# Kernel optimization log

Measured on AMD Instinct MI355X. Metric: run time of the kernel, lower is better.

Reference implementation:

```python
import jax, jax.numpy as jnp
import numpy as np

RHO, MU, DT = 1.0, 0.1, 4.0
AX_X, AX_Y = -1, -2  # x = last axis, y = second-to-last


def first_derivative(f, ax, scheme):
    # unit grid spacing; boundary wrap is irrelevant since [1:-1,1:-1] is sliced off
    if scheme == 'left':
        return f - jnp.roll(f, 1, ax)
    if scheme == 'right':
        return jnp.roll(f, -1, ax) - f
    return 0.5 * (jnp.roll(f, -1, ax) - jnp.roll(f, 1, ax))  # central


def vel_map(f, ax, side):
    # staggered-grid interpolation of velocity to neighboring face
    if side == 'left':
        return 0.5 * (f + jnp.roll(f, 1, ax))
    return 0.5 * (f + jnp.roll(f, -1, ax))


def laplacian(f):
    return (jnp.roll(f, 1, AX_X) + jnp.roll(f, -1, AX_X)
            + jnp.roll(f, 1, AX_Y) + jnp.roll(f, -1, AX_Y) - 4.0 * f)


def setup_inputs() -> dict:
    key = jax.random.key(0)
    k1, k2, k3, k4 = jax.random.split(key, 4)
    B, H, W = 8, 1024, 1024
    return {
        'v_old': jax.random.normal(k1, (B, 2, H, W), dtype=jnp.float32),
        'v_new': jax.random.normal(k2, (B, 2, H, W), dtype=jnp.float32),
        'p_new': jax.random.normal(k3, (B, 1, H, W), dtype=jnp.float32),
        'flow_mask_mac': jax.random.randint(k4, (B, 1, H, W), 0, 2).astype(jnp.int32),
    }


def reference(v_old, v_new, p_new, flow_mask_mac):
    mask = flow_mask_mac.astype(v_old.dtype)
    v = 0.5 * (v_new + v_old)  # integration == 'imex'

    u_old, w_old = v_old[:, 0:1], v_old[:, 1:2]
    u_new, w_new = v_new[:, 0:1], v_new[:, 1:2]
    u, w = v[:, 0:1], v[:, 1:2]

    # x-momentum residual (channel 1)
    res_x = mask * (RHO * ((w_new - w_old) / DT
                           + w * first_derivative(w, AX_X, 'central')
                           + 0.5 * (vel_map(u, AX_X, 'left') * first_derivative(w, AX_Y, 'left')
                                    + vel_map(u, AX_X, 'right') * first_derivative(w, AX_Y, 'right')))
                    + first_derivative(p_new, AX_X, 'left')
                    - MU * laplacian(w))

    # y-momentum residual (channel 0)
    res_y = mask * (RHO * ((u_new - u_old) / DT
                           + u * first_derivative(u, AX_Y, 'central')
                           + 0.5 * (vel_map(w, AX_Y, 'left') * first_derivative(u, AX_X, 'left')
                                    + vel_map(w, AX_Y, 'right') * first_derivative(u, AX_X, 'right')))
                    + first_derivative(p_new, AX_Y, 'left')
                    - MU * laplacian(u))

    loss_x = jnp.mean(jnp.square(res_x)[:, :, 1:-1, 1:-1], axis=(1, 2, 3))
    loss_y = jnp.mean(jnp.square(res_y)[:, :, 1:-1, 1:-1], axis=(1, 2, 3))
    return loss_x + loss_y  # shape [B]
```

## Files before the change

### kernel.cpp

```cpp
#include <hip/hip_runtime.h>


#define NS_H 1024
#define NS_W 1024
#define RPB 2
#define PAIRS ((NS_H - 2) / RPB)
#define PARTS_PER_B PAIRS

__device__ __forceinline__ float4 ld4(const float* p) { return *(const float4*)p; }
__device__ __forceinline__ float4 avg4(float4 a, float4 b) {
    return make_float4(0.5f*(a.x+b.x), 0.5f*(a.y+b.y), 0.5f*(a.z+b.z), 0.5f*(a.w+b.w));
}
__device__ __forceinline__ float4 sub4(float4 a, float4 b) {
    return make_float4(a.x-b.x, a.y-b.y, a.z-b.z, a.w-b.w);
}

__global__ __launch_bounds__(256, 3) void ns_loss_partial(
    const float* __restrict__ v_old,
    const float* __restrict__ v_new,
    const float* __restrict__ p,
    const int*   __restrict__ mask,
    float* __restrict__ ws)
{
    const int blk = blockIdx.x;
    const int b   = blk / PAIRS;
    const int pr  = blk % PAIRS;
    const int y   = 1 + pr * RPB;

    const size_t hw = (size_t)NS_H * NS_W;
    const float* uo = v_old + (size_t)b * 2 * hw;
    const float* wo = uo + hw;
    const float* un = v_new + (size_t)b * 2 * hw;
    const float* wn = un + hw;
    const float* pb = p    + (size_t)b * hw;
    const int*   mb = mask + (size_t)b * hw;

    const int tid  = (int)threadIdx.x;
    const int lane = tid & 63;
    const int x0   = tid * 4;
    const bool has_r = (x0 + 4 < NS_W);
    const bool seamL = (lane == 0) && (x0 > 0);
    const bool seamR = (lane == 63) && has_r;

    const int rm  = (y - 1) * NS_W;
    const int rc  = y * NS_W;
    const int rp  = rc + NS_W;
    const int rpp = rp + NS_W;

    float4 un_m = ld4(un + rm  + x0), uo_m = ld4(uo + rm  + x0);
    float4 un_c = ld4(un + rc  + x0), uo_c = ld4(uo + rc  + x0);
    float4 un_p = ld4(un + rp  + x0), uo_p = ld4(uo + rp  + x0);
    float4 un_q = ld4(un + rpp + x0), uo_q = ld4(uo + rpp + x0);
    float4 wn_m = ld4(wn + rm  + x0), wo_m = ld4(wo + rm  + x0);
    float4 wn_c = ld4(wn + rc  + x0), wo_c = ld4(wo + rc  + x0);
    float4 wn_p = ld4(wn + rp  + x0), wo_p = ld4(wo + rp  + x0);
    float4 wn_q = ld4(wn + rpp + x0), wo_q = ld4(wo + rpp + x0);
    float4 p_m4 = ld4(pb + rm + x0);
    float4 p_c4 = ld4(pb + rc + x0);
    float4 p_p4 = ld4(pb + rp + x0);
    int4   m_c4 = *(const int4*)(mb + rc + x0);
    int4   m_p4 = *(const int4*)(mb + rp + x0);

    float4 u_m = avg4(un_m, uo_m), u_c = avg4(un_c, uo_c);
    float4 u_p = avg4(un_p, uo_p), u_q = avg4(un_q, uo_q);
    float4 w_m = avg4(wn_m, wo_m), w_c = avg4(wn_c, wo_c);
    float4 w_p = avg4(wn_p, wo_p), w_q = avg4(wn_q, wo_q);
    float4 du_c = sub4(un_c, uo_c), du_p = sub4(un_p, uo_p);
    float4 dw_c = sub4(wn_c, wo_c), dw_p = sub4(wn_p, wo_p);

    float ul_c = __shfl_up(u_c.w, 1), wl_c = __shfl_up(w_c.w, 1);
    float ul_p = __shfl_up(u_p.w, 1), wl_p = __shfl_up(w_p.w, 1);
    float pl_c = __shfl_up(p_c4.w, 1), pl_p = __shfl_up(p_p4.w, 1);
    if (seamL) {
        ul_c = 0.5f * (un[rc + x0 - 1] + uo[rc + x0 - 1]);
        wl_c = 0.5f * (wn[rc + x0 - 1] + wo[rc + x0 - 1]);
        ul_p = 0.5f * (un[rp + x0 - 1] + uo[rp + x0 - 1]);
        wl_p = 0.5f * (wn[rp + x0 - 1] + wo[rp + x0 - 1]);
        pl_c = pb[rc + x0 - 1];
        pl_p = pb[rp + x0 - 1];
    }
    float ur_c = __shfl_down(u_c.x, 1), wr_c = __shfl_down(w_c.x, 1);
    float ur_p = __shfl_down(u_p.x, 1), wr_p = __shfl_down(w_p.x, 1);
    if (seamR) {
        ur_c = 0.5f * (un[rc + x0 + 4] + uo[rc + x0 + 4]);
        wr_c = 0.5f * (wn[rc + x0 + 4] + wo[rc + x0 + 4]);
        ur_p = 0.5f * (un[rp + x0 + 4] + uo[rp + x0 + 4]);
        wr_p = 0.5f * (wn[rp + x0 + 4] + wo[rp + x0 + 4]);
    }
    if (!has_r) { ur_c = 0.f; wr_c = 0.f; ur_p = 0.f; wr_p = 0.f; }

    float acc = 0.f;

    {
        const float uc[6]  = {ul_c, u_c.x, u_c.y, u_c.z, u_c.w, ur_c};
        const float wcv[6] = {wl_c, w_c.x, w_c.y, w_c.z, w_c.w, wr_c};
        const float uym[4] = {u_m.x, u_m.y, u_m.z, u_m.w};
        const float uyp[4] = {u_p.x, u_p.y, u_p.z, u_p.w};
        const float wym[4] = {w_m.x, w_m.y, w_m.z, w_m.w};
        const float wyp[4] = {w_p.x, w_p.y, w_p.z, w_p.w};
        const float du[4]  = {du_c.x, du_c.y, du_c.z, du_c.w};
        const float dw[4]  = {dw_c.x, dw_c.y, dw_c.z, dw_c.w};
        const float pcv[5] = {pl_c, p_c4.x, p_c4.y, p_c4.z, p_c4.w};
        const float pym[4] = {p_m4.x, p_m4.y, p_m4.z, p_m4.w};
        const int   mm[4]  = {m_c4.x, m_c4.y, m_c4.z, m_c4.w};

        #pragma unroll
        for (int j = 0; j < 4; ++j) {
            const int x = x0 + j;
            const float m = (x >= 1 && x <= NS_W - 2) ? (float)mm[j] : 0.f;
            const float u_cc = uc[j+1],  u_xm = uc[j],  u_xp = uc[j+2];
            const float w_cc = wcv[j+1], w_xm = wcv[j], w_xp = wcv[j+2];

            float res_x =
                dw[j] * 0.25f
              + w_cc * 0.5f * (w_xp - w_xm)
              + 0.5f * ( 0.5f * (u_cc + u_xm) * (w_cc   - wym[j])
                       + 0.5f * (u_cc + u_xp) * (wyp[j] - w_cc  ) )
              + (pcv[j+1] - pcv[j])
              - 0.1f * (w_xm + w_xp + wym[j] + wyp[j] - 4.f * w_cc);

            float res_y =
                du[j] * 0.25f
              + u_cc * 0.5f * (uyp[j] - uym[j])
              + 0.5f * ( 0.5f * (w_cc + wym[j]) * (u_cc - u_xm)
                       + 0.5f * (w_cc + wyp[j]) * (u_xp - u_cc) )
              + (pcv[j+1] - pym[j])
              - 0.1f * (u_xm + u_xp + uym[j] + uyp[j] - 4.f * u_cc);

            acc += m * (res_x * res_x + res_y * res_y);
        }
    }

    {
        const float uc[6]  = {ul_p, u_p.x, u_p.y, u_p.z, u_p.w, ur_p};
        const float wcv[6] = {wl_p, w_p.x, w_p.y, w_p.z, w_p.w, wr_p};
        const float uym[4] = {u_c.x, u_c.y, u_c.z, u_c.w};
        const float uyp[4] = {u_q.x, u_q.y, u_q.z, u_q.w};
        const float wym[4] = {w_c.x, w_c.y, w_c.z, w_c.w};
        const float wyp[4] = {w_q.x, w_q.y, w_q.z, w_q.w};
        const float du[4]  = {du_p.x, du_p.y, du_p.z, du_p.w};
        const float dw[4]  = {dw_p.x, dw_p.y, dw_p.z, dw_p.w};
        const float pcv[5] = {pl_p, p_p4.x, p_p4.y, p_p4.z, p_p4.w};
        const float pym[4] = {p_c4.x, p_c4.y, p_c4.z, p_c4.w};
        const int   mm[4]  = {m_p4.x, m_p4.y, m_p4.z, m_p4.w};

        #pragma unroll
        for (int j = 0; j < 4; ++j) {
            const int x = x0 + j;
            const float m = (x >= 1 && x <= NS_W - 2) ? (float)mm[j] : 0.f;
            const float u_cc = uc[j+1],  u_xm = uc[j],  u_xp = uc[j+2];
            const float w_cc = wcv[j+1], w_xm = wcv[j], w_xp = wcv[j+2];

            float res_x =
                dw[j] * 0.25f
              + w_cc * 0.5f * (w_xp - w_xm)
              + 0.5f * ( 0.5f * (u_cc + u_xm) * (w_cc   - wym[j])
                       + 0.5f * (u_cc + u_xp) * (wyp[j] - w_cc  ) )
              + (pcv[j+1] - pcv[j])
              - 0.1f * (w_xm + w_xp + wym[j] + wyp[j] - 4.f * w_cc);

            float res_y =
                du[j] * 0.25f
              + u_cc * 0.5f * (uyp[j] - uym[j])
              + 0.5f * ( 0.5f * (w_cc + wym[j]) * (u_cc - u_xm)
                       + 0.5f * (w_cc + wyp[j]) * (u_xp - u_cc) )
              + (pcv[j+1] - pym[j])
              - 0.1f * (u_xm + u_xp + uym[j] + uyp[j] - 4.f * u_cc);

            acc += m * (res_x * res_x + res_y * res_y);
        }
    }

    #pragma unroll
    for (int off = 32; off > 0; off >>= 1)
        acc += __shfl_down(acc, off);

    __shared__ float smem[4];
    const int wid = tid >> 6;
    if (lane == 0) smem[wid] = acc;
    __syncthreads();

    if (tid == 0)
        ws[blk] = smem[0] + smem[1] + smem[2] + smem[3];
}

__global__ __launch_bounds__(256) void ns_loss_reduce(
    const float* __restrict__ ws, float* __restrict__ out)
{
    const int b = blockIdx.x;
    float acc = 0.f;
    for (int i = threadIdx.x; i < PARTS_PER_B; i += 256)
        acc += ws[b * PARTS_PER_B + i];

    #pragma unroll
    for (int off = 32; off > 0; off >>= 1)
        acc += __shfl_down(acc, off);

    __shared__ float smem[4];
    const int lane = threadIdx.x & 63;
    const int wid  = threadIdx.x >> 6;
    if (lane == 0) smem[wid] = acc;
    __syncthreads();

    if (threadIdx.x == 0) {
        const float inv = 1.0f / ((float)(NS_H - 2) * (float)(NS_W - 2));
        out[b] = (smem[0] + smem[1] + smem[2] + smem[3]) * inv;
    }
}

extern "C" void kernel_launch(void* const* d_in, const int* in_sizes, int n_in,
                              void* d_out, int out_size, void* d_ws, size_t ws_size,
                              hipStream_t stream) {
    const float* v_old = (const float*)d_in[0];
    const float* v_new = (const float*)d_in[1];
    const float* p_new = (const float*)d_in[2];
    const int*   msk   = (const int*)d_in[3];
    float* out = (float*)d_out;
    float* ws  = (float*)d_ws;

    const int B = out_size;

    ns_loss_partial<<<dim3(B * PAIRS), dim3(256), 0, stream>>>(v_old, v_new, p_new, msk, ws);
    ns_loss_reduce<<<dim3(B), dim3(256), 0, stream>>>(ws, out);
}
```

Measured before the change: 199.7 us.

## Stream eight rows per block with rolling register window and one-row prefetch

Each block now processes a strip of eight rows, sliding u/w/p/mask registers down one row per iteration instead of reloading neighbor rows for every pair of rows. The next row is prefetched while the current row is computed. This removes the redundant halo-row global reads of the two-row-per-block scheme and shrinks the partial-sum workspace. In exchange it launches far fewer blocks, which reduces parallelism and latency hiding, and adds a loop-carried dependency on loads.

```diff
diff --git a/kernel.cpp b/kernel.cpp
--- a/kernel.cpp
+++ b/kernel.cpp
@@ -3,11 +3,12 @@
 
 #define NS_H 1024
 #define NS_W 1024
-#define RPB 2
-#define PAIRS ((NS_H - 2) / RPB)
-#define PARTS_PER_B PAIRS
+#define RY   8
+#define NBY  128
+#define PARTS_PER_B NBY
 
 __device__ __forceinline__ float4 ld4(const float* p) { return *(const float4*)p; }
+__device__ __forceinline__ int4  ld4i(const int* p)   { return *(const int4*)p; }
 __device__ __forceinline__ float4 avg4(float4 a, float4 b) {
     return make_float4(0.5f*(a.x+b.x), 0.5f*(a.y+b.y), 0.5f*(a.z+b.z), 0.5f*(a.w+b.w));
 }
@@ -23,9 +24,10 @@
     float* __restrict__ ws)
 {
     const int blk = blockIdx.x;
-    const int b   = blk / PAIRS;
-    const int pr  = blk % PAIRS;
-    const int y   = 1 + pr * RPB;
+    const int b   = blk / NBY;
+    const int cy  = blk % NBY;
+    const int y0  = 1 + cy * RY;
+    const int ny  = min(RY, (NS_H - 1) - y0);
 
     const size_t hw = (size_t)NS_H * NS_W;
     const float* uo = v_old + (size_t)b * 2 * hw;
@@ -38,136 +40,128 @@
     const int tid  = (int)threadIdx.x;
     const int lane = tid & 63;
     const int x0   = tid * 4;
-    const bool has_r = (x0 + 4 < NS_W);
-    const bool seamL = (lane == 0) && (x0 > 0);
-    const bool seamR = (lane == 63) && has_r;
-
-    const int rm  = (y - 1) * NS_W;
-    const int rc  = y * NS_W;
-    const int rp  = rc + NS_W;
-    const int rpp = rp + NS_W;
-
-    float4 un_m = ld4(un + rm  + x0), uo_m = ld4(uo + rm  + x0);
-    float4 un_c = ld4(un + rc  + x0), uo_c = ld4(uo + rc  + x0);
-    float4 un_p = ld4(un + rp  + x0), uo_p = ld4(uo + rp  + x0);
-    float4 un_q = ld4(un + rpp + x0), uo_q = ld4(uo + rpp + x0);
-    float4 wn_m = ld4(wn + rm  + x0), wo_m = ld4(wo + rm  + x0);
-    float4 wn_c = ld4(wn + rc  + x0), wo_c = ld4(wo + rc  + x0);
-    float4 wn_p = ld4(wn + rp  + x0), wo_p = ld4(wo + rp  + x0);
-    float4 wn_q = ld4(wn + rpp + x0), wo_q = ld4(wo + rpp + x0);
-    float4 p_m4 = ld4(pb + rm + x0);
-    float4 p_c4 = ld4(pb + rc + x0);
-    float4 p_p4 = ld4(pb + rp + x0);
-    int4   m_c4 = *(const int4*)(mb + rc + x0);
-    int4   m_p4 = *(const int4*)(mb + rp + x0);
-
-    float4 u_m = avg4(un_m, uo_m), u_c = avg4(un_c, uo_c);
-    float4 u_p = avg4(un_p, uo_p), u_q = avg4(un_q, uo_q);
-    float4 w_m = avg4(wn_m, wo_m), w_c = avg4(wn_c, wo_c);
-    float4 w_p = avg4(wn_p, wo_p), w_q = avg4(wn_q, wo_q);
-    float4 du_c = sub4(un_c, uo_c), du_p = sub4(un_p, uo_p);
-    float4 dw_c = sub4(wn_c, wo_c), dw_p = sub4(wn_p, wo_p);
-
-    float ul_c = __shfl_up(u_c.w, 1), wl_c = __shfl_up(w_c.w, 1);
-    float ul_p = __shfl_up(u_p.w, 1), wl_p = __shfl_up(w_p.w, 1);
-    float pl_c = __shfl_up(p_c4.w, 1), pl_p = __shfl_up(p_p4.w, 1);
+    const bool seamL = (lane == 0)  && (x0 > 0);
+    const bool seamR = (lane == 63) && (x0 + 4 < NS_W);
+
+    const int off_m = (y0 - 1) * NS_W + x0;
+    const int off_c = off_m + NS_W;
+    const int off_p = off_c + NS_W;
+    const int off_q = off_p + NS_W;
+
+    float4 t0 = ld4(un + off_m), t1 = ld4(uo + off_m);
+    float4 t2 = ld4(wn + off_m), t3 = ld4(wo + off_m);
+    float4 t4 = ld4(un + off_c), t5 = ld4(uo + off_c);
+    float4 t6 = ld4(wn + off_c), t7 = ld4(wo + off_c);
+    float4 t8 = ld4(un + off_p), t9 = ld4(uo + off_p);
+    float4 ta = ld4(wn + off_p), tb = ld4(wo + off_p);
+    float4 p_m4 = ld4(pb + off_m);
+    float4 p_c4 = ld4(pb + off_c);
+    int4   m_c4 = ld4i(mb + off_c);
+
+    float4 u_m = avg4(t0, t1), w_m = avg4(t2, t3);
+    float4 u_c = avg4(t4, t5), du_c = sub4(t4, t5);
+    float4 w_c = avg4(t6, t7), dw_c = sub4(t6, t7);
+    float4 u_p = avg4(t8, t9), du_p = sub4(t8, t9);
+    float4 w_p = avg4(ta, tb), dw_p = sub4(ta, tb);
+
+    float s_ul = 0.f, s_wl = 0.f, s_pl = 0.f, s_ur = 0.f, s_wr = 0.f;
     if (seamL) {
-        ul_c = 0.5f * (un[rc + x0 - 1] + uo[rc + x0 - 1]);
-        wl_c = 0.5f * (wn[rc + x0 - 1] + wo[rc + x0 - 1]);
-        ul_p = 0.5f * (un[rp + x0 - 1] + uo[rp + x0 - 1]);
-        wl_p = 0.5f * (wn[rp + x0 - 1] + wo[rp + x0 - 1]);
-        pl_c = pb[rc + x0 - 1];
-        pl_p = pb[rp + x0 - 1];
-    }
-    float ur_c = __shfl_down(u_c.x, 1), wr_c = __shfl_down(w_c.x, 1);
-    float ur_p = __shfl_down(u_p.x, 1), wr_p = __shfl_down(w_p.x, 1);
+        s_ul = 0.5f * (un[off_c - 1] + uo[off_c - 1]);
+        s_wl = 0.5f * (wn[off_c - 1] + wo[off_c - 1]);
+        s_pl = pb[off_c - 1];
+    }
     if (seamR) {
-        ur_c = 0.5f * (un[rc + x0 + 4] + uo[rc + x0 + 4]);
-        wr_c = 0.5f * (wn[rc + x0 + 4] + wo[rc + x0 + 4]);
-        ur_p = 0.5f * (un[rp + x0 + 4] + uo[rp + x0 + 4]);
-        wr_p = 0.5f * (wn[rp + x0 + 4] + wo[rp + x0 + 4]);
-    }
-    if (!has_r) { ur_c = 0.f; wr_c = 0.f; ur_p = 0.f; wr_p = 0.f; }
+        s_ur = 0.5f * (un[off_c + 4] + uo[off_c + 4]);
+        s_wr = 0.5f * (wn[off_c + 4] + wo[off_c + 4]);
+    }
+
+    float4 f_un = ld4(un + off_q), f_uo = ld4(uo + off_q);
+    float4 f_wn = ld4(wn + off_q), f_wo = ld4(wo + off_q);
+    float4 f_p  = ld4(pb + off_p);
+    int4   f_m  = ld4i(mb + off_p);
+    float f_ul = 0.f, f_wl = 0.f, f_pl = 0.f, f_ur = 0.f, f_wr = 0.f;
+    if (seamL) {
+        f_ul = 0.5f * (un[off_p - 1] + uo[off_p - 1]);
+        f_wl = 0.5f * (wn[off_p - 1] + wo[off_p - 1]);
+        f_pl = pb[off_p - 1];
+    }
+    if (seamR) {
+        f_ur = 0.5f * (un[off_p + 4] + uo[off_p + 4]);
+        f_wr = 0.5f * (wn[off_p + 4] + wo[off_p + 4]);
+    }
 
     float acc = 0.f;
 
-    {
-        const float uc[6]  = {ul_c, u_c.x, u_c.y, u_c.z, u_c.w, ur_c};
-        const float wcv[6] = {wl_c, w_c.x, w_c.y, w_c.z, w_c.w, wr_c};
-        const float uym[4] = {u_m.x, u_m.y, u_m.z, u_m.w};
-        const float uyp[4] = {u_p.x, u_p.y, u_p.z, u_p.w};
-        const float wym[4] = {w_m.x, w_m.y, w_m.z, w_m.w};
-        const float wyp[4] = {w_p.x, w_p.y, w_p.z, w_p.w};
-        const float du[4]  = {du_c.x, du_c.y, du_c.z, du_c.w};
-        const float dw[4]  = {dw_c.x, dw_c.y, dw_c.z, dw_c.w};
-        const float pcv[5] = {pl_c, p_c4.x, p_c4.y, p_c4.z, p_c4.w};
-        const float pym[4] = {p_m4.x, p_m4.y, p_m4.z, p_m4.w};
-        const int   mm[4]  = {m_c4.x, m_c4.y, m_c4.z, m_c4.w};
-
-        #pragma unroll
-        for (int j = 0; j < 4; ++j) {
-            const int x = x0 + j;
-            const float m = (x >= 1 && x <= NS_W - 2) ? (float)mm[j] : 0.f;
-            const float u_cc = uc[j+1],  u_xm = uc[j],  u_xp = uc[j+2];
-            const float w_cc = wcv[j+1], w_xm = wcv[j], w_xp = wcv[j+2];
-
-            float res_x =
-                dw[j] * 0.25f
-              + w_cc * 0.5f * (w_xp - w_xm)
-              + 0.5f * ( 0.5f * (u_cc + u_xm) * (w_cc   - wym[j])
-                       + 0.5f * (u_cc + u_xp) * (wyp[j] - w_cc  ) )
-              + (pcv[j+1] - pcv[j])
-              - 0.1f * (w_xm + w_xp + wym[j] + wyp[j] - 4.f * w_cc);
-
-            float res_y =
-                du[j] * 0.25f
-              + u_cc * 0.5f * (uyp[j] - uym[j])
-              + 0.5f * ( 0.5f * (w_cc + wym[j]) * (u_cc - u_xm)
-                       + 0.5f * (w_cc + wyp[j]) * (u_xp - u_cc) )
-              + (pcv[j+1] - pym[j])
-              - 0.1f * (u_xm + u_xp + uym[j] + uyp[j] - 4.f * u_cc);
-
-            acc += m * (res_x * res_x + res_y * res_y);
+    for (int r = 0; r < ny; ++r) {
+        float ul = __shfl_up(u_c.w, 1);   if (lane == 0)  ul = s_ul;
+        float wl = __shfl_up(w_c.w, 1);   if (lane == 0)  wl = s_wl;
+        float pl = __shfl_up(p_c4.w, 1);  if (lane == 0)  pl = s_pl;
+        float ur = __shfl_down(u_c.x, 1); if (lane == 63) ur = s_ur;
+        float wr = __shfl_down(w_c.x, 1); if (lane == 63) wr = s_wr;
+
+        {
+            const float uc[6]  = {ul, u_c.x, u_c.y, u_c.z, u_c.w, ur};
+            const float wcv[6] = {wl, w_c.x, w_c.y, w_c.z, w_c.w, wr};
+            const float uym[4] = {u_m.x, u_m.y, u_m.z, u_m.w};
+            const float uyp[4] = {u_p.x, u_p.y, u_p.z, u_p.w};
+            const float wym[4] = {w_m.x, w_m.y, w_m.z, w_m.w};
+            const float wyp[4] = {w_p.x, w_p.y, w_p.z, w_p.w};
+            const float du[4]  = {du_c.x, du_c.y, du_c.z, du_c.w};
+            const float dw[4]  = {dw_c.x, dw_c.y, dw_c.z, dw_c.w};
+            const float pcv[5] = {pl, p_c4.x, p_c4.y, p_c4.z, p_c4.w};
+            const float pym[4] = {p_m4.x, p_m4.y, p_m4.z, p_m4.w};
+            const int   mm[4]  = {m_c4.x, m_c4.y, m_c4.z, m_c4.w};
+
+            #pragma unroll
+            for (int j = 0; j < 4; ++j) {
+                const int x = x0 + j;
+                const float m = (x >= 1 && x <= NS_W - 2) ? (float)mm[j] : 0.f;
+                const float u_cc = uc[j+1],  u_xm = uc[j],  u_xp = uc[j+2];
+                const float w_cc = wcv[j+1], w_xm = wcv[j], w_xp = wcv[j+2];
+
+                float res_x =
+                    dw[j] * 0.25f
+                  + w_cc * 0.5f * (w_xp - w_xm)
+                  + 0.5f * ( 0.5f * (u_cc + u_xm) * (w_cc   - wym[j])
+                           + 0.5f * (u_cc + u_xp) * (wyp[j] - w_cc  ) )
+                  + (pcv[j+1] - pcv[j])
+                  - 0.1f * (w_xm + w_xp + wym[j] + wyp[j] - 4.f * w_cc);
+
+                float res_y =
+                    du[j] * 0.25f
+                  + u_cc * 0.5f * (uyp[j] - uym[j])
+                  + 0.5f * ( 0.5f * (w_cc + wym[j]) * (u_cc - u_xm)
+                           + 0.5f * (w_cc + wyp[j]) * (u_xp - u_cc) )
+                  + (pcv[j+1] - pym[j])
+                  - 0.1f * (u_xm + u_xp + uym[j] + uyp[j] - 4.f * u_cc);
+
+                acc += m * (res_x * res_x + res_y * res_y);
+            }
         }
-    }
-
-    {
-        const float uc[6]  = {ul_p, u_p.x, u_p.y, u_p.z, u_p.w, ur_p};
-        const float wcv[6] = {wl_p, w_p.x, w_p.y, w_p.z, w_p.w, wr_p};
-        const float uym[4] = {u_c.x, u_c.y, u_c.z, u_c.w};
-        const float uyp[4] = {u_q.x, u_q.y, u_q.z, u_q.w};
-        const float wym[4] = {w_c.x, w_c.y, w_c.z, w_c.w};
-        const float wyp[4] = {w_q.x, w_q.y, w_q.z, w_q.w};
-        const float du[4]  = {du_p.x, du_p.y, du_p.z, du_p.w};
-        const float dw[4]  = {dw_p.x, dw_p.y, dw_p.z, dw_p.w};
-        const float pcv[5] = {pl_p, p_p4.x, p_p4.y, p_p4.z, p_p4.w};
-        const float pym[4] = {p_c4.x, p_c4.y, p_c4.z, p_c4.w};
-        const int   mm[4]  = {m_p4.x, m_p4.y, m_p4.z, m_p4.w};
-
-        #pragma unroll
-        for (int j = 0; j < 4; ++j) {
-            const int x = x0 + j;
-            const float m = (x >= 1 && x <= NS_W - 2) ? (float)mm[j] : 0.f;
-            const float u_cc = uc[j+1],  u_xm = uc[j],  u_xp = uc[j+2];
-            const float w_cc = wcv[j+1], w_xm = wcv[j], w_xp = wcv[j+2];
-
-            float res_x =
-                dw[j] * 0.25f
-              + w_cc * 0.5f * (w_xp - w_xm)
-              + 0.5f * ( 0.5f * (u_cc + u_xm) * (w_cc   - wym[j])
-                       + 0.5f * (u_cc + u_xp) * (wyp[j] - w_cc  ) )
-              + (pcv[j+1] - pcv[j])
-              - 0.1f * (w_xm + w_xp + wym[j] + wyp[j] - 4.f * w_cc);
-
-            float res_y =
-                du[j] * 0.25f
-              + u_cc * 0.5f * (uyp[j] - uym[j])
-              + 0.5f * ( 0.5f * (w_cc + wym[j]) * (u_cc - u_xm)
-                       + 0.5f * (w_cc + wyp[j]) * (u_xp - u_cc) )
-              + (pcv[j+1] - pym[j])
-              - 0.1f * (u_xm + u_xp + uym[j] + uyp[j] - 4.f * u_cc);
-
-            acc += m * (res_x * res_x + res_y * res_y);
+
+        u_m = u_c;  w_m = w_c;
+        u_c = u_p;  w_c = w_p;  du_c = du_p;  dw_c = dw_p;
+        u_p = avg4(f_un, f_uo); du_p = sub4(f_un, f_uo);
+        w_p = avg4(f_wn, f_wo); dw_p = sub4(f_wn, f_wo);
+        p_m4 = p_c4; p_c4 = f_p; m_c4 = f_m;
+        s_ul = f_ul; s_wl = f_wl; s_pl = f_pl; s_ur = f_ur; s_wr = f_wr;
+
+        int row_q = y0 + r + 3; if (row_q > NS_H - 1) row_q = NS_H - 1;
+        int row_n = y0 + r + 2; if (row_n > NS_H - 1) row_n = NS_H - 1;
+        const int off_q2 = row_q * NS_W + x0;
+        const int off_n  = row_n * NS_W + x0;
+        f_un = ld4(un + off_q2); f_uo = ld4(uo + off_q2);
+        f_wn = ld4(wn + off_q2); f_wo = ld4(wo + off_q2);
+        f_p  = ld4(pb + off_n);
+        f_m  = ld4i(mb + off_n);
+        if (seamL) {
+            f_ul = 0.5f * (un[off_n - 1] + uo[off_n - 1]);
+            f_wl = 0.5f * (wn[off_n - 1] + wo[off_n - 1]);
+            f_pl = pb[off_n - 1];
+        }
+        if (seamR) {
+            f_ur = 0.5f * (un[off_n + 4] + uo[off_n + 4]);
+            f_wr = 0.5f * (wn[off_n + 4] + wo[off_n + 4]);
         }
     }
 
@@ -220,6 +214,6 @@
 
     const int B = out_size;
 
-    ns_loss_partial<<<dim3(B * PAIRS), dim3(256), 0, stream>>>(v_old, v_new, p_new, msk, ws);
+    ns_loss_partial<<<dim3(B * NBY), dim3(256), 0, stream>>>(v_old, v_new, p_new, msk, ws);
     ns_loss_reduce<<<dim3(B), dim3(256), 0, stream>>>(ws, out);
 }
```

Result: slower. 207.5 us (+3.9%).

## Exchange wavefront seam values via LDS and swizzle block order across batches

Applied to the files above, without the earlier changes.

Seam lanes at wavefront boundaries used to issue extra scalar global loads to fetch neighbour values. They now get them from a small shared-memory edge array filled by the adjacent wavefronts, at the cost of an added __syncthreads. Block IDs are remapped so consecutive blocks cycle through the batch index, which changes how traffic spreads across memory channels and XCDs. A sched_barrier is placed after the vector loads so they are all issued before any compute is scheduled.

```diff
diff --git a/kernel.cpp b/kernel.cpp
--- a/kernel.cpp
+++ b/kernel.cpp
@@ -8,6 +8,7 @@
 #define PARTS_PER_B PAIRS
 
 __device__ __forceinline__ float4 ld4(const float* p) { return *(const float4*)p; }
+__device__ __forceinline__ int4  ld4i(const int* p)   { return *(const int4*)p; }
 __device__ __forceinline__ float4 avg4(float4 a, float4 b) {
     return make_float4(0.5f*(a.x+b.x), 0.5f*(a.y+b.y), 0.5f*(a.z+b.z), 0.5f*(a.w+b.w));
 }
@@ -22,10 +23,11 @@
     const int*   __restrict__ mask,
     float* __restrict__ ws)
 {
-    const int blk = blockIdx.x;
-    const int b   = blk / PAIRS;
-    const int pr  = blk % PAIRS;
-    const int y   = 1 + pr * RPB;
+    const int blkp = blockIdx.x;
+    const int lg   = (blkp & 7) * PAIRS + (blkp >> 3);
+    const int b    = lg / PAIRS;
+    const int pr   = lg % PAIRS;
+    const int y    = 1 + pr * RPB;
 
     const size_t hw = (size_t)NS_H * NS_W;
     const float* uo = v_old + (size_t)b * 2 * hw;
@@ -37,10 +39,9 @@
 
     const int tid  = (int)threadIdx.x;
     const int lane = tid & 63;
+    const int wid  = tid >> 6;
     const int x0   = tid * 4;
     const bool has_r = (x0 + 4 < NS_W);
-    const bool seamL = (lane == 0) && (x0 > 0);
-    const bool seamR = (lane == 63) && has_r;
 
     const int rm  = (y - 1) * NS_W;
     const int rc  = y * NS_W;
@@ -58,8 +59,9 @@
     float4 p_m4 = ld4(pb + rm + x0);
     float4 p_c4 = ld4(pb + rc + x0);
     float4 p_p4 = ld4(pb + rp + x0);
-    int4   m_c4 = *(const int4*)(mb + rc + x0);
-    int4   m_p4 = *(const int4*)(mb + rp + x0);
+    int4   m_c4 = ld4i(mb + rc + x0);
+    int4   m_p4 = ld4i(mb + rp + x0);
+    __builtin_amdgcn_sched_barrier(0);
 
     float4 u_m = avg4(un_m, uo_m), u_c = avg4(un_c, uo_c);
     float4 u_p = avg4(un_p, uo_p), u_q = avg4(un_q, uo_q);
@@ -68,24 +70,29 @@
     float4 du_c = sub4(un_c, uo_c), du_p = sub4(un_p, uo_p);
     float4 dw_c = sub4(wn_c, wo_c), dw_p = sub4(wn_p, wo_p);
 
-    float ul_c = __shfl_up(u_c.w, 1), wl_c = __shfl_up(w_c.w, 1);
-    float ul_p = __shfl_up(u_p.w, 1), wl_p = __shfl_up(w_p.w, 1);
+    __shared__ float edge[4][10];
+    if (lane == 63) {
+        edge[wid][0] = u_c.w;  edge[wid][1] = w_c.w;  edge[wid][2] = p_c4.w;
+        edge[wid][3] = u_p.w;  edge[wid][4] = w_p.w;  edge[wid][5] = p_p4.w;
+    }
+    if (lane == 0) {
+        edge[wid][6] = u_c.x;  edge[wid][7] = w_c.x;
+        edge[wid][8] = u_p.x;  edge[wid][9] = w_p.x;
+    }
+    __syncthreads();
+
+    float ul_c = __shfl_up(u_c.w, 1),  wl_c = __shfl_up(w_c.w, 1);
+    float ul_p = __shfl_up(u_p.w, 1),  wl_p = __shfl_up(w_p.w, 1);
     float pl_c = __shfl_up(p_c4.w, 1), pl_p = __shfl_up(p_p4.w, 1);
-    if (seamL) {
-        ul_c = 0.5f * (un[rc + x0 - 1] + uo[rc + x0 - 1]);
-        wl_c = 0.5f * (wn[rc + x0 - 1] + wo[rc + x0 - 1]);
-        ul_p = 0.5f * (un[rp + x0 - 1] + uo[rp + x0 - 1]);
-        wl_p = 0.5f * (wn[rp + x0 - 1] + wo[rp + x0 - 1]);
-        pl_c = pb[rc + x0 - 1];
-        pl_p = pb[rp + x0 - 1];
+    if (lane == 0 && wid > 0) {
+        ul_c = edge[wid-1][0]; wl_c = edge[wid-1][1]; pl_c = edge[wid-1][2];
+        ul_p = edge[wid-1][3]; wl_p = edge[wid-1][4]; pl_p = edge[wid-1][5];
     }
     float ur_c = __shfl_down(u_c.x, 1), wr_c = __shfl_down(w_c.x, 1);
     float ur_p = __shfl_down(u_p.x, 1), wr_p = __shfl_down(w_p.x, 1);
-    if (seamR) {
-        ur_c = 0.5f * (un[rc + x0 + 4] + uo[rc + x0 + 4]);
-        wr_c = 0.5f * (wn[rc + x0 + 4] + wo[rc + x0 + 4]);
-        ur_p = 0.5f * (un[rp + x0 + 4] + uo[rp + x0 + 4]);
-        wr_p = 0.5f * (wn[rp + x0 + 4] + wo[rp + x0 + 4]);
+    if (lane == 63 && wid < 3) {
+        ur_c = edge[wid+1][6]; wr_c = edge[wid+1][7];
+        ur_p = edge[wid+1][8]; wr_p = edge[wid+1][9];
     }
     if (!has_r) { ur_c = 0.f; wr_c = 0.f; ur_p = 0.f; wr_p = 0.f; }
 
@@ -176,12 +183,11 @@
         acc += __shfl_down(acc, off);
 
     __shared__ float smem[4];
-    const int wid = tid >> 6;
     if (lane == 0) smem[wid] = acc;
     __syncthreads();
 
     if (tid == 0)
-        ws[blk] = smem[0] + smem[1] + smem[2] + smem[3];
+        ws[lg] = smem[0] + smem[1] + smem[2] + smem[3];
 }
 
 __global__ __launch_bounds__(256) void ns_loss_reduce(
```

Result: no change. 200.4 us (+0.4%).
